# Kernel tuning notes

Hardware: AMD Instinct MI355X
Metric: run time of the kernel (lower is better)

## Reference

```python
import jax, jax.numpy as jnp
import numpy as np

TAU = 2.0        # spikingjelly LIFNode default tau
ALPHA = 4.0      # sigmoid surrogate alpha (spikingjelly default)
NUM_HEADS = 8
CHUNK = 2

@jax.custom_vjp
def heaviside(x):
    return (x >= 0).astype(x.dtype)

def _h_fwd(x):
    return heaviside(x), x

def _h_bwd(x, g):
    s = jax.nn.sigmoid(ALPHA * x)
    return (g * ALPHA * s * (1.0 - s),)

heaviside.defvjp(_h_fwd, _h_bwd)

def lif(x, v_th):
    # multi-step LIF: v <- v + (x - v)/tau ; spike = H(v - v_th) ; hard reset to 0
    def step(v, xt):
        v = v + (xt - v) / TAU
        s = heaviside(v - v_th)
        return v * (1.0 - s), s
    _, spikes = jax.lax.scan(step, jnp.zeros_like(x[0]), x)
    return spikes

def bn(x, p, eps=1e-5):
    # eval-mode BatchNorm1d over channel dim C of [T,B,C,V]; p = [gamma,beta,mean,var] each [C]
    g, b, m, v = p[0], p[1], p[2], p[3]
    scale = g * jax.lax.rsqrt(v + eps)
    return (x - m[:, None]) * scale[:, None] + b[:, None]

def setup_inputs() -> dict:
    key = jax.random.key(0)
    T, B, C, V = 8, 16, 256, 1024
    ks = jax.random.split(key, 10)
    def mk_bn(k):
        k1, k2, k3, k4 = jax.random.split(k, 4)
        return jnp.stack([
            jax.random.uniform(k1, (C,)) + 0.5,          # gamma
            0.1 * jax.random.normal(k2, (C,)),           # beta
            0.1 * jax.random.normal(k3, (C,)),           # running mean
            jax.random.uniform(k4, (C,)) * 0.5 + 0.5,    # running var (>0)
        ])
    w_scale = C ** -0.5
    return {
        "x": jax.random.normal(ks[0], (T, B, C, V), jnp.float32),
        "q_w": w_scale * jax.random.normal(ks[1], (C, C), jnp.float32),
        "k_w": w_scale * jax.random.normal(ks[2], (C, C), jnp.float32),
        "v_w": w_scale * jax.random.normal(ks[3], (C, C), jnp.float32),
        "proj_w": w_scale * jax.random.normal(ks[4], (C, C), jnp.float32),
        "proj_b": 0.01 * jax.random.normal(ks[5], (C,), jnp.float32),
        "bn_q": mk_bn(ks[6]),
        "bn_k": mk_bn(ks[7]),
        "bn_v": mk_bn(ks[8]),
        "bn_proj": mk_bn(ks[9]),
    }

def reference(x, q_w, k_w, v_w, proj_w, proj_b, bn_q, bn_k, bn_v, bn_proj):
    T, B, C, V = x.shape
    H = NUM_HEADS
    D = C // H
    N = V
    NC = T // CHUNK
    identity = x

    xs = lif(x, 1.0)  # shortcut_lif

    def branch(w, bnp):
        y = jnp.einsum('oc,tbcv->tbov', w, xs)   # 1x1 conv
        y = lif(bn(y, bnp), 1.0)
        # [T,B,C,V] -> [T,B,H,N,D]
        return y.transpose(0, 1, 3, 2).reshape(T, B, N, H, D).transpose(0, 1, 3, 2, 4)

    q = branch(q_w, bn_q)
    k = branch(k_w, bn_k)
    v = branch(v_w, bn_v)

    def chunk(t):
        # [T,B,H,N,D] -> [NC,B,H,CHUNK*N,D]
        return (t.reshape(NC, CHUNK, B, H, N, D)
                 .transpose(0, 2, 3, 1, 4, 5)
                 .reshape(NC, B, H, CHUNK * N, D))

    qc, kc, vc = chunk(q), chunk(k), chunk(v)
    attn = jnp.einsum('nbhld,nbhle->nbhde', kc, vc) * (1.0 / N)  # [NC,B,H,D,D]
    out = jnp.einsum('nbhld,nbhde->nbhle', qc, attn)             # [NC,B,H,CHUNK*N,D]
    out = (out.reshape(NC, B, H, CHUNK, N, D)
              .transpose(0, 3, 1, 2, 4, 5)
              .reshape(T, B, H, N, D))

    y = out.transpose(0, 1, 2, 4, 3).reshape(T, B, C, N)  # [T,B,H,D,N] -> [T,B,C,N]
    y = lif(y, 0.5)  # attn_lif
    y = jnp.einsum('oc,tbcv->tbov', proj_w, y) + proj_b[None, None, :, None]
    y = bn(y, bn_proj)
    return y + identity, v
```

## Files before the change

kernel.cpp:

```cpp
#include <hip/hip_runtime.h>
#include <hip/hip_bf16.h>
#include <math.h>

typedef __bf16 bf16_t;
typedef __bf16 bf16x8 __attribute__((ext_vector_type(8)));
typedef __bf16 bf16x4 __attribute__((ext_vector_type(4)));
typedef float  f32x4  __attribute__((ext_vector_type(4)));

#define T_ 8
#define B_ 16
#define C_ 256
#define V_ 1024
#define H_ 8
#define D_ 32

#define MFMA __builtin_amdgcn_mfma_f32_16x16x32_bf16

__global__ __launch_bounds__(256) void k0_split(const float* __restrict__ W,
                                                bf16_t* __restrict__ S0,
                                                bf16_t* __restrict__ S1,
                                                bf16_t* __restrict__ S2)
{
    int i = (blockIdx.x * 256 + threadIdx.x) * 4;
    float4 w = *(const float4*)(W + i);
    float wv[4] = {w.x, w.y, w.z, w.w};
    bf16x4 s0, s1, s2;
#pragma unroll
    for (int j = 0; j < 4; j++) {
        bf16_t a = (bf16_t)wv[j];
        float r1 = wv[j] - (float)a;
        bf16_t b = (bf16_t)r1;
        float r2 = r1 - (float)b;
        bf16_t c = (bf16_t)r2;
        s0[j] = a; s1[j] = b; s2[j] = c;
    }
    *(bf16x4*)(S0 + i) = s0;
    *(bf16x4*)(S1 + i) = s1;
    *(bf16x4*)(S2 + i) = s2;
}

__global__ __launch_bounds__(256) void k1_lif_tr(const float* __restrict__ x,
                                                 bf16_t* __restrict__ xsT)
{
    __shared__ bf16_t tile[64 * 72];
    const int v0 = blockIdx.x * 64, c0 = blockIdx.y * 64, b = blockIdx.z;
    const int tid = threadIdx.x;
    const int cc = tid >> 2, v16 = (tid & 3) * 16;
    const int vr = tid >> 2, c16 = (tid & 3) * 16;
    float mem[16];
#pragma unroll
    for (int j = 0; j < 16; j++) mem[j] = 0.0f;

    for (int t = 0; t < T_; t++) {
        const float* xp = x + (((size_t)(t * B_ + b) * C_ + (c0 + cc)) * V_ + v0 + v16);
        float xv[16];
#pragma unroll
        for (int q = 0; q < 4; q++) {
            float4 f = *(const float4*)(xp + q * 4);
            xv[q * 4 + 0] = f.x; xv[q * 4 + 1] = f.y;
            xv[q * 4 + 2] = f.z; xv[q * 4 + 3] = f.w;
        }
#pragma unroll
        for (int j = 0; j < 16; j++) {
            float m = mem[j];
            float d = xv[j] - m;
            m = m + d * 0.5f;
            float s = (m >= 1.0f) ? 1.0f : 0.0f;
            tile[(v16 + j) * 72 + cc] = (bf16_t)s;
            mem[j] = (s != 0.0f) ? 0.0f : m;
        }
        __syncthreads();
        bf16_t* op = xsT + (((size_t)(t * B_ + b) * V_ + (v0 + vr)) * C_ + c0 + c16);
        *(bf16x8*)op       = *(const bf16x8*)&tile[vr * 72 + c16];
        *(bf16x8*)(op + 8) = *(const bf16x8*)&tile[vr * 72 + c16 + 8];
        __syncthreads();
    }
}

template <int ORIENT>
__global__ __launch_bounds__(256, 2) void k_branch(const bf16_t* __restrict__ Wsp,
                                                   const float* __restrict__ bnp,
                                                   const bf16_t* __restrict__ xsT,
                                                   bf16_t* __restrict__ outp, float vth)
{
    __shared__ bf16_t Wl[3][64 * 40];
    __shared__ bf16_t Xl[8][64 * 40];
    __shared__ float bsc[64], bmn[64], bbt[64];
    const int v0 = blockIdx.x * 64, o0 = blockIdx.y * 64, b = blockIdx.z;
    const int tid = threadIdx.x;
    const int w = tid >> 6, l = tid & 63, lq = l >> 4, lr = l & 15;
    const int msub = (w >> 1) * 32, nsub = (w & 1) * 32;

    if (tid < 64) {
        int o = o0 + tid;
        float g = bnp[o], be = bnp[C_ + o];
        float mn = bnp[2 * C_ + o], vr2 = bnp[3 * C_ + o];
        bsc[tid] = g * (1.0f / sqrtf(vr2 + 1e-5f));
        bmn[tid] = mn; bbt[tid] = be;
    }

    f32x4 acc[8][4];
#pragma unroll
    for (int t = 0; t < 8; t++)
#pragma unroll
        for (int i = 0; i < 4; i++) acc[t][i] = (f32x4){0.f, 0.f, 0.f, 0.f};

    for (int kq = 0; kq < 8; kq++) {
        __syncthreads();
#pragma unroll
        for (int i = 0; i < 3; i++) {
            int ch = tid + i * 256;
            int lvl = ch >> 8, rem = ch & 255;
            int row = rem >> 2, col8 = (rem & 3) * 8;
            *(bf16x8*)&Wl[lvl][row * 40 + col8] =
                *(const bf16x8*)&Wsp[lvl * 65536 + (o0 + row) * 256 + kq * 32 + col8];
        }
#pragma unroll
        for (int i = 0; i < 8; i++) {
            int ch = tid + i * 256;
            int tt = ch >> 8, rem = ch & 255;
            int row = rem >> 2, col8 = (rem & 3) * 8;
            *(bf16x8*)&Xl[tt][row * 40 + col8] =
                *(const bf16x8*)&xsT[((size_t)(tt * B_ + b) * V_ + v0 + row) * C_ + kq * 32 + col8];
        }
        __syncthreads();

        bf16x8 aw0[3], aw1[3];
#pragma unroll
        for (int lvl = 0; lvl < 3; lvl++) {
            aw0[lvl] = *(const bf16x8*)&Wl[lvl][(msub + lr) * 40 + lq * 8];
            aw1[lvl] = *(const bf16x8*)&Wl[lvl][(msub + 16 + lr) * 40 + lq * 8];
        }
#pragma unroll
        for (int t = 0; t < 8; t++) {
            bf16x8 b0 = *(const bf16x8*)&Xl[t][(nsub + lr) * 40 + lq * 8];
            bf16x8 b1 = *(const bf16x8*)&Xl[t][(nsub + 16 + lr) * 40 + lq * 8];
#pragma unroll
            for (int lvl = 0; lvl < 3; lvl++) {
                if (ORIENT == 0) {
                    acc[t][0] = MFMA(aw0[lvl], b0, acc[t][0], 0, 0, 0);
                    acc[t][1] = MFMA(aw0[lvl], b1, acc[t][1], 0, 0, 0);
                    acc[t][2] = MFMA(aw1[lvl], b0, acc[t][2], 0, 0, 0);
                    acc[t][3] = MFMA(aw1[lvl], b1, acc[t][3], 0, 0, 0);
                } else {
                    acc[t][0] = MFMA(b0, aw0[lvl], acc[t][0], 0, 0, 0);
                    acc[t][1] = MFMA(b1, aw0[lvl], acc[t][1], 0, 0, 0);
                    acc[t][2] = MFMA(b0, aw1[lvl], acc[t][2], 0, 0, 0);
                    acc[t][3] = MFMA(b1, aw1[lvl], acc[t][3], 0, 0, 0);
                }
            }
        }
    }

    float mem[4][4];
#pragma unroll
    for (int st = 0; st < 4; st++)
#pragma unroll
        for (int r = 0; r < 4; r++) mem[st][r] = 0.0f;
#pragma unroll
    for (int t = 0; t < 8; t++) {
#pragma unroll
        for (int st = 0; st < 4; st++) {
            int mi = st >> 1, ni = st & 1;
#pragma unroll
            for (int r = 0; r < 4; r++) {
                int m, n;
                if (ORIENT == 0) {
                    m = msub + mi * 16 + lq * 4 + r;
                    n = nsub + ni * 16 + lr;
                } else {
                    m = msub + mi * 16 + lr;
                    n = nsub + ni * 16 + lq * 4 + r;
                }
                float y = (acc[t][st][r] - bmn[m]) * bsc[m] + bbt[m];
                float mm = mem[st][r];
                mm = mm + (y - mm) * 0.5f;
                float s = (mm >= vth) ? 1.0f : 0.0f;
                size_t idx = ORIENT
                    ? (((size_t)(t * B_ + b) * V_ + (v0 + n)) * C_ + (o0 + m))
                    : (((size_t)(t * B_ + b) * C_ + (o0 + m)) * V_ + (v0 + n));
                outp[idx] = (bf16_t)s;
                mem[st][r] = (s != 0.0f) ? 0.0f : mm;
            }
        }
    }
}

__global__ __launch_bounds__(256) void k_attn(const bf16_t* __restrict__ vc,
                                              const bf16_t* __restrict__ kc,
                                              bf16_t* __restrict__ ahi,
                                              bf16_t* __restrict__ alo)
{
    __shared__ float red[3][64][20];
    const int fid = blockIdx.x;
    const int h = fid & 7, b = (fid >> 3) & 15, nc = fid >> 7;
    const int tid = threadIdx.x, w = tid >> 6, l = tid & 63, lq = l >> 4, lr = l & 15;
    f32x4 acc[4];
#pragma unroll
    for (int i = 0; i < 4; i++) acc[i] = (f32x4){0.f, 0.f, 0.f, 0.f};
    for (int ss = 0; ss < 16; ss++) {
        int s = w * 16 + ss;
        int t = nc * 2 + (s >> 5);
        int n0 = (s & 31) * 32;
        size_t rb = ((size_t)(t * B_ + b) * C_ + h * D_ + lr) * V_ + n0 + lq * 8;
        bf16x8 a0 = *(const bf16x8*)&vc[rb];
        bf16x8 a1 = *(const bf16x8*)&vc[rb + (size_t)16 * V_];
        bf16x8 b0 = *(const bf16x8*)&kc[rb];
        bf16x8 b1 = *(const bf16x8*)&kc[rb + (size_t)16 * V_];
        acc[0] = MFMA(a0, b0, acc[0], 0, 0, 0);
        acc[1] = MFMA(a0, b1, acc[1], 0, 0, 0);
        acc[2] = MFMA(a1, b0, acc[2], 0, 0, 0);
        acc[3] = MFMA(a1, b1, acc[3], 0, 0, 0);
    }
    if (w) {
#pragma unroll
        for (int st = 0; st < 4; st++)
            *(f32x4*)&red[w - 1][l][st * 4] = acc[st];
    }
    __syncthreads();
    if (w == 0) {
#pragma unroll
        for (int st = 0; st < 4; st++)
#pragma unroll
            for (int i = 0; i < 3; i++)
                acc[st] += *(const f32x4*)&red[i][l][st * 4];

        size_t ob = (size_t)fid * 1024;
#pragma unroll
        for (int st = 0; st < 4; st++) {
            int ei = st >> 1, di = st & 1;
#pragma unroll
            for (int r = 0; r < 4; r++) {
                int e = ei * 16 + lq * 4 + r;
                int d = di * 16 + lr;
                float val = acc[st][r] * (1.0f / 1024.0f);
                bf16_t hi = (bf16_t)val;
                float lo = val - (float)hi;
                ahi[ob + e * 32 + d] = hi;
                alo[ob + e * 32 + d] = (bf16_t)lo;
            }
        }
    }
}

__global__ __launch_bounds__(256) void k_attn_out(const bf16_t* __restrict__ qT,
                                                  const bf16_t* __restrict__ ahi,
                                                  const bf16_t* __restrict__ alo,
                                                  bf16_t* __restrict__ y3T)
{
    const int tid = threadIdx.x, w = tid >> 6, l = tid & 63, lq = l >> 4, lr = l & 15;
    const int n0 = blockIdx.x * 64 + (w >> 1) * 32;
    const int h = blockIdx.y * 2 + (w & 1);
    const int b = blockIdx.z;
    float mem[4][4];
#pragma unroll
    for (int st = 0; st < 4; st++)
#pragma unroll
        for (int r = 0; r < 4; r++) mem[st][r] = 0.0f;

    for (int t = 0; t < T_; t++) {
        int nc = t >> 1;
        const bf16_t* qp = qT + ((size_t)(t * B_ + b) * V_ + n0 + lr) * C_ + h * D_ + lq * 8;
        bf16x8 a0 = *(const bf16x8*)qp;
        bf16x8 a1 = *(const bf16x8*)(qp + 16 * C_);
        size_t ab = ((size_t)(nc * B_ + b) * H_ + h) * 1024;
        bf16x8 bh0 = *(const bf16x8*)&ahi[ab + lr * 32 + lq * 8];
        bf16x8 bh1 = *(const bf16x8*)&ahi[ab + (16 + lr) * 32 + lq * 8];
        bf16x8 bl0 = *(const bf16x8*)&alo[ab + lr * 32 + lq * 8];
        bf16x8 bl1 = *(const bf16x8*)&alo[ab + (16 + lr) * 32 + lq * 8];
#pragma unroll
        for (int st = 0; st < 4; st++) {
            int mi = st >> 1, ni = st & 1;
            f32x4 z = (f32x4){0.f, 0.f, 0.f, 0.f};
            z = MFMA(mi ? a1 : a0, ni ? bh1 : bh0, z, 0, 0, 0);
            z = MFMA(mi ? a1 : a0, ni ? bl1 : bl0, z, 0, 0, 0);
#pragma unroll
            for (int r = 0; r < 4; r++) {
                int n = n0 + mi * 16 + lq * 4 + r;
                int e = ni * 16 + lr;
                float mm = mem[st][r];
                mm = mm + (z[r] - mm) * 0.5f;
                float s = (mm >= 0.5f) ? 1.0f : 0.0f;
                y3T[((size_t)(t * B_ + b) * V_ + n) * C_ + h * D_ + e] = (bf16_t)s;
                mem[st][r] = (s != 0.0f) ? 0.0f : mm;
            }
        }
    }
}

__global__ __launch_bounds__(256, 2) void k_proj(const bf16_t* __restrict__ Wsp,
                                                 const float* __restrict__ pb,
                                                 const float* __restrict__ bnp,
                                                 const bf16_t* __restrict__ y3T,
                                                 const float* __restrict__ x,
                                                 float* __restrict__ out0)
{
    __shared__ bf16_t Wl[3][64 * 40];
    __shared__ bf16_t Xl[8][64 * 40];
    __shared__ float bsc[64], bmn[64], bbt[64], bbi[64];
    const int v0 = blockIdx.x * 64, o0 = blockIdx.y * 64, b = blockIdx.z;
    const int tid = threadIdx.x;
    const int w = tid >> 6, l = tid & 63, lq = l >> 4, lr = l & 15;
    const int msub = (w >> 1) * 32, nsub = (w & 1) * 32;

    if (tid < 64) {
        int o = o0 + tid;
        float g = bnp[o], be = bnp[C_ + o];
        float mn = bnp[2 * C_ + o], vr2 = bnp[3 * C_ + o];
        bsc[tid] = g * (1.0f / sqrtf(vr2 + 1e-5f));
        bmn[tid] = mn; bbt[tid] = be; bbi[tid] = pb[o];
    }

    f32x4 acc[8][4];
#pragma unroll
    for (int t = 0; t < 8; t++)
#pragma unroll
        for (int i = 0; i < 4; i++) acc[t][i] = (f32x4){0.f, 0.f, 0.f, 0.f};

    for (int kq = 0; kq < 8; kq++) {
        __syncthreads();
#pragma unroll
        for (int i = 0; i < 3; i++) {
            int ch = tid + i * 256;
            int lvl = ch >> 8, rem = ch & 255;
            int row = rem >> 2, col8 = (rem & 3) * 8;
            *(bf16x8*)&Wl[lvl][row * 40 + col8] =
                *(const bf16x8*)&Wsp[lvl * 65536 + (o0 + row) * 256 + kq * 32 + col8];
        }
#pragma unroll
        for (int i = 0; i < 8; i++) {
            int ch = tid + i * 256;
            int tt = ch >> 8, rem = ch & 255;
            int row = rem >> 2, col8 = (rem & 3) * 8;
            *(bf16x8*)&Xl[tt][row * 40 + col8] =
                *(const bf16x8*)&y3T[((size_t)(tt * B_ + b) * V_ + v0 + row) * C_ + kq * 32 + col8];
        }
        __syncthreads();

        bf16x8 aw0[3], aw1[3];
#pragma unroll
        for (int lvl = 0; lvl < 3; lvl++) {
            aw0[lvl] = *(const bf16x8*)&Wl[lvl][(msub + lr) * 40 + lq * 8];
            aw1[lvl] = *(const bf16x8*)&Wl[lvl][(msub + 16 + lr) * 40 + lq * 8];
        }
#pragma unroll
        for (int t = 0; t < 8; t++) {
            bf16x8 b0 = *(const bf16x8*)&Xl[t][(nsub + lr) * 40 + lq * 8];
            bf16x8 b1 = *(const bf16x8*)&Xl[t][(nsub + 16 + lr) * 40 + lq * 8];
#pragma unroll
            for (int lvl = 0; lvl < 3; lvl++) {
                acc[t][0] = MFMA(aw0[lvl], b0, acc[t][0], 0, 0, 0);
                acc[t][1] = MFMA(aw0[lvl], b1, acc[t][1], 0, 0, 0);
                acc[t][2] = MFMA(aw1[lvl], b0, acc[t][2], 0, 0, 0);
                acc[t][3] = MFMA(aw1[lvl], b1, acc[t][3], 0, 0, 0);
            }
        }
    }

#pragma unroll
    for (int t = 0; t < 8; t++) {
#pragma unroll
        for (int st = 0; st < 4; st++) {
            int mi = st >> 1, ni = st & 1;
#pragma unroll
            for (int r = 0; r < 4; r++) {
                int m = msub + mi * 16 + lq * 4 + r;
                int n = nsub + ni * 16 + lr;
                size_t idx = ((size_t)(t * B_ + b) * C_ + (o0 + m)) * V_ + (v0 + n);
                float y = acc[t][st][r] + bbi[m];
                y = (y - bmn[m]) * bsc[m] + bbt[m];
                y += x[idx];
                out0[idx] = y;
            }
        }
    }
}

__global__ __launch_bounds__(256) void k_vout(const bf16_t* __restrict__ vc,
                                              float* __restrict__ out1)
{
    __shared__ bf16_t tl[32 * 136];
    const int n0 = blockIdx.x * 128;
    const int f = blockIdx.y;
    const int tb = f >> 3, h = f & 7;
    const int tid = threadIdx.x;
    {
        int d = tid >> 3, nn = (tid & 7) * 16;
        const bf16_t* vp = vc + ((size_t)tb * C_ + h * D_ + d) * V_ + n0 + nn;
        *(bf16x8*)&tl[d * 136 + nn]     = *(const bf16x8*)vp;
        *(bf16x8*)&tl[d * 136 + nn + 8] = *(const bf16x8*)(vp + 8);
    }
    __syncthreads();
    {
        int n = tid >> 1, d16 = (tid & 1) * 16;
        float* op = out1 + (size_t)f * (V_ * D_) + (size_t)(n0 + n) * D_ + d16;
#pragma unroll
        for (int q = 0; q < 4; q++) {
            float4 o;
            o.x = (float)tl[(d16 + q * 4 + 0) * 136 + n];
            o.y = (float)tl[(d16 + q * 4 + 1) * 136 + n];
            o.z = (float)tl[(d16 + q * 4 + 2) * 136 + n];
            o.w = (float)tl[(d16 + q * 4 + 3) * 136 + n];
            *(float4*)(op + q * 4) = o;
        }
    }
}

extern "C" void kernel_launch(void* const* d_in, const int* in_sizes, int n_in,
                              void* d_out, int out_size, void* d_ws, size_t ws_size,
                              hipStream_t stream)
{
    const float* x    = (const float*)d_in[0];
    const float* q_w  = (const float*)d_in[1];
    const float* k_w  = (const float*)d_in[2];
    const float* v_w  = (const float*)d_in[3];
    const float* pw   = (const float*)d_in[4];
    const float* pb   = (const float*)d_in[5];
    const float* bn_q = (const float*)d_in[6];
    const float* bn_k = (const float*)d_in[7];
    const float* bn_v = (const float*)d_in[8];
    const float* bn_p = (const float*)d_in[9];

    char* ws = (char*)d_ws;
    bf16_t* xsT  = (bf16_t*)(ws);
    bf16_t* vc   = (bf16_t*)(ws + ((size_t)64 << 20));
    bf16_t* ahi  = (bf16_t*)(ws + ((size_t)128 << 20));
    bf16_t* alo  = (bf16_t*)(ws + ((size_t)129 << 20));
    bf16_t* wspq = (bf16_t*)(ws + ((size_t)130 << 20));
    bf16_t* wspk = wspq + 3 * 65536;
    bf16_t* wspv = wspk + 3 * 65536;
    bf16_t* wspp = wspv + 3 * 65536;
    bf16_t* y3T  = xsT;

    float* outf = (float*)d_out;
    bf16_t* qT = (bf16_t*)d_out;
    bf16_t* kc = (bf16_t*)((char*)d_out + ((size_t)64 << 20));

    k0_split<<<dim3(64), 256, 0, stream>>>(q_w, wspq, wspq + 65536, wspq + 131072);
    k0_split<<<dim3(64), 256, 0, stream>>>(k_w, wspk, wspk + 65536, wspk + 131072);
    k0_split<<<dim3(64), 256, 0, stream>>>(v_w, wspv, wspv + 65536, wspv + 131072);
    k0_split<<<dim3(64), 256, 0, stream>>>(pw,  wspp, wspp + 65536, wspp + 131072);

    k1_lif_tr   <<<dim3(16, 4, 16),  256, 0, stream>>>(x, xsT);
    k_branch<1> <<<dim3(16, 4, 16),  256, 0, stream>>>(wspq, bn_q, xsT, qT, 1.0f);
    k_branch<0> <<<dim3(16, 4, 16),  256, 0, stream>>>(wspk, bn_k, xsT, kc, 1.0f);
    k_branch<0> <<<dim3(16, 4, 16),  256, 0, stream>>>(wspv, bn_v, xsT, vc, 1.0f);
    k_attn      <<<dim3(512),        256, 0, stream>>>(vc, kc, ahi, alo);
    k_attn_out  <<<dim3(16, 4, 16),  256, 0, stream>>>(qT, ahi, alo, y3T);
    k_proj      <<<dim3(16, 4, 16),  256, 0, stream>>>(wspp, pb, bn_p, y3T, x, outf);
    k_vout      <<<dim3(8, 1024),    256, 0, stream>>>(vc, outf + (size_t)33554432);
}
```

Baseline: 712.6 us.

## Prefetch GEMM tiles into registers, fuse v output into branch, merge split kernels

The branch and proj GEMM kernels now load the next K-slice of weights and activations into registers while the current slice is computed from shared memory, overlapping global loads with MFMA work. The v branch kernel also writes the fp32 v output directly through a shared-memory transpose, which removes the separate k_vout pass that re-read vc. The four weight-split launches are merged into one. The cost is higher register pressure from holding 11 bf16x8 staging vectors under launch_bounds(256,2), plus extra syncs inside the v kernel's per-timestep epilogue.

```diff
diff --git a/kernel.cpp b/kernel.cpp
--- a/kernel.cpp
+++ b/kernel.cpp
@@ -16,12 +16,18 @@
 
 #define MFMA __builtin_amdgcn_mfma_f32_16x16x32_bf16
 
-__global__ __launch_bounds__(256) void k0_split(const float* __restrict__ W,
-                                                bf16_t* __restrict__ S0,
-                                                bf16_t* __restrict__ S1,
-                                                bf16_t* __restrict__ S2)
-{
-    int i = (blockIdx.x * 256 + threadIdx.x) * 4;
+__global__ __launch_bounds__(256) void k0_split4(const float* __restrict__ W0,
+                                                 const float* __restrict__ W1,
+                                                 const float* __restrict__ W2,
+                                                 const float* __restrict__ W3,
+                                                 bf16_t* __restrict__ S)
+{
+    const int mat = blockIdx.x >> 6;
+    const float* W = (mat == 0) ? W0 : (mat == 1) ? W1 : (mat == 2) ? W2 : W3;
+    bf16_t* S0 = S + (size_t)mat * 3 * 65536;
+    bf16_t* S1 = S0 + 65536;
+    bf16_t* S2 = S0 + 131072;
+    int i = ((blockIdx.x & 63) * 256 + threadIdx.x) * 4;
     float4 w = *(const float4*)(W + i);
     float wv[4] = {w.x, w.y, w.z, w.w};
     bf16x4 s0, s1, s2;
@@ -77,11 +83,12 @@
     }
 }
 
-template <int ORIENT>
+template <int ORIENT, int VOUT>
 __global__ __launch_bounds__(256, 2) void k_branch(const bf16_t* __restrict__ Wsp,
                                                    const float* __restrict__ bnp,
                                                    const bf16_t* __restrict__ xsT,
-                                                   bf16_t* __restrict__ outp, float vth)
+                                                   bf16_t* __restrict__ outp, float vth,
+                                                   float* __restrict__ out1)
 {
     __shared__ bf16_t Wl[3][64 * 40];
     __shared__ bf16_t Xl[8][64 * 40];
@@ -105,25 +112,50 @@
 #pragma unroll
         for (int i = 0; i < 4; i++) acc[t][i] = (f32x4){0.f, 0.f, 0.f, 0.f};
 
+    bf16x8 wst[3], xst[8];
+#pragma unroll
+    for (int i = 0; i < 3; i++) {
+        int ch = tid + i * 256, lvl = ch >> 8, rem = ch & 255;
+        int row = rem >> 2, col8 = (rem & 3) * 8;
+        wst[i] = *(const bf16x8*)&Wsp[lvl * 65536 + (o0 + row) * 256 + col8];
+    }
+#pragma unroll
+    for (int i = 0; i < 8; i++) {
+        int ch = tid + i * 256, tt = ch >> 8, rem = ch & 255;
+        int row = rem >> 2, col8 = (rem & 3) * 8;
+        xst[i] = *(const bf16x8*)&xsT[((size_t)(tt * B_ + b) * V_ + v0 + row) * C_ + col8];
+    }
+
     for (int kq = 0; kq < 8; kq++) {
         __syncthreads();
 #pragma unroll
         for (int i = 0; i < 3; i++) {
-            int ch = tid + i * 256;
-            int lvl = ch >> 8, rem = ch & 255;
+            int ch = tid + i * 256, lvl = ch >> 8, rem = ch & 255;
             int row = rem >> 2, col8 = (rem & 3) * 8;
-            *(bf16x8*)&Wl[lvl][row * 40 + col8] =
-                *(const bf16x8*)&Wsp[lvl * 65536 + (o0 + row) * 256 + kq * 32 + col8];
+            *(bf16x8*)&Wl[lvl][row * 40 + col8] = wst[i];
         }
 #pragma unroll
         for (int i = 0; i < 8; i++) {
-            int ch = tid + i * 256;
-            int tt = ch >> 8, rem = ch & 255;
+            int ch = tid + i * 256, tt = ch >> 8, rem = ch & 255;
             int row = rem >> 2, col8 = (rem & 3) * 8;
-            *(bf16x8*)&Xl[tt][row * 40 + col8] =
-                *(const bf16x8*)&xsT[((size_t)(tt * B_ + b) * V_ + v0 + row) * C_ + kq * 32 + col8];
-        }
-        __syncthreads();
+            *(bf16x8*)&Xl[tt][row * 40 + col8] = xst[i];
+        }
+        __syncthreads();
+        if (kq < 7) {
+            int kc8 = (kq + 1) * 32;
+#pragma unroll
+            for (int i = 0; i < 3; i++) {
+                int ch = tid + i * 256, lvl = ch >> 8, rem = ch & 255;
+                int row = rem >> 2, col8 = (rem & 3) * 8;
+                wst[i] = *(const bf16x8*)&Wsp[lvl * 65536 + (o0 + row) * 256 + kc8 + col8];
+            }
+#pragma unroll
+            for (int i = 0; i < 8; i++) {
+                int ch = tid + i * 256, tt = ch >> 8, rem = ch & 255;
+                int row = rem >> 2, col8 = (rem & 3) * 8;
+                xst[i] = *(const bf16x8*)&xsT[((size_t)(tt * B_ + b) * V_ + v0 + row) * C_ + kc8 + col8];
+            }
+        }
 
         bf16x8 aw0[3], aw1[3];
 #pragma unroll
@@ -152,6 +184,8 @@
         }
     }
 
+    bf16_t* tl = (bf16_t*)Xl;
+    if (VOUT) __syncthreads();
     float mem[4][4];
 #pragma unroll
     for (int st = 0; st < 4; st++)
@@ -181,7 +215,25 @@
                     : (((size_t)(t * B_ + b) * C_ + (o0 + m)) * V_ + (v0 + n));
                 outp[idx] = (bf16_t)s;
                 mem[st][r] = (s != 0.0f) ? 0.0f : mm;
-            }
+                if (VOUT) tl[n * 66 + m] = (bf16_t)s;
+            }
+        }
+        if (VOUT) {
+            __syncthreads();
+            int nn = tid & 63, ho = tid >> 6;
+            int h = (o0 >> 5) + (ho >> 1), d16 = (ho & 1) * 16;
+            float* op = out1 + ((size_t)((t * B_ + b) * H_ + h)) * (V_ * D_)
+                             + (size_t)(v0 + nn) * D_ + d16;
+#pragma unroll
+            for (int q2 = 0; q2 < 4; q2++) {
+                float4 o4;
+                o4.x = (float)tl[nn * 66 + ho * 16 + q2 * 4 + 0];
+                o4.y = (float)tl[nn * 66 + ho * 16 + q2 * 4 + 1];
+                o4.z = (float)tl[nn * 66 + ho * 16 + q2 * 4 + 2];
+                o4.w = (float)tl[nn * 66 + ho * 16 + q2 * 4 + 3];
+                *(float4*)(op + q2 * 4) = o4;
+            }
+            __syncthreads();
         }
     }
 }
@@ -317,25 +369,50 @@
 #pragma unroll
         for (int i = 0; i < 4; i++) acc[t][i] = (f32x4){0.f, 0.f, 0.f, 0.f};
 
+    bf16x8 wst[3], xst[8];
+#pragma unroll
+    for (int i = 0; i < 3; i++) {
+        int ch = tid + i * 256, lvl = ch >> 8, rem = ch & 255;
+        int row = rem >> 2, col8 = (rem & 3) * 8;
+        wst[i] = *(const bf16x8*)&Wsp[lvl * 65536 + (o0 + row) * 256 + col8];
+    }
+#pragma unroll
+    for (int i = 0; i < 8; i++) {
+        int ch = tid + i * 256, tt = ch >> 8, rem = ch & 255;
+        int row = rem >> 2, col8 = (rem & 3) * 8;
+        xst[i] = *(const bf16x8*)&y3T[((size_t)(tt * B_ + b) * V_ + v0 + row) * C_ + col8];
+    }
+
     for (int kq = 0; kq < 8; kq++) {
         __syncthreads();
 #pragma unroll
         for (int i = 0; i < 3; i++) {
-            int ch = tid + i * 256;
-            int lvl = ch >> 8, rem = ch & 255;
+            int ch = tid + i * 256, lvl = ch >> 8, rem = ch & 255;
             int row = rem >> 2, col8 = (rem & 3) * 8;
-            *(bf16x8*)&Wl[lvl][row * 40 + col8] =
-                *(const bf16x8*)&Wsp[lvl * 65536 + (o0 + row) * 256 + kq * 32 + col8];
+            *(bf16x8*)&Wl[lvl][row * 40 + col8] = wst[i];
         }
 #pragma unroll
         for (int i = 0; i < 8; i++) {
-            int ch = tid + i * 256;
-            int tt = ch >> 8, rem = ch & 255;
+            int ch = tid + i * 256, tt = ch >> 8, rem = ch & 255;
             int row = rem >> 2, col8 = (rem & 3) * 8;
-            *(bf16x8*)&Xl[tt][row * 40 + col8] =
-                *(const bf16x8*)&y3T[((size_t)(tt * B_ + b) * V_ + v0 + row) * C_ + kq * 32 + col8];
-        }
-        __syncthreads();
+            *(bf16x8*)&Xl[tt][row * 40 + col8] = xst[i];
+        }
+        __syncthreads();
+        if (kq < 7) {
+            int kc8 = (kq + 1) * 32;
+#pragma unroll
+            for (int i = 0; i < 3; i++) {
+                int ch = tid + i * 256, lvl = ch >> 8, rem = ch & 255;
+                int row = rem >> 2, col8 = (rem & 3) * 8;
+                wst[i] = *(const bf16x8*)&Wsp[lvl * 65536 + (o0 + row) * 256 + kc8 + col8];
+            }
+#pragma unroll
+            for (int i = 0; i < 8; i++) {
+                int ch = tid + i * 256, tt = ch >> 8, rem = ch & 255;
+                int row = rem >> 2, col8 = (rem & 3) * 8;
+                xst[i] = *(const bf16x8*)&y3T[((size_t)(tt * B_ + b) * V_ + v0 + row) * C_ + kc8 + col8];
+            }
+        }
 
         bf16x8 aw0[3], aw1[3];
 #pragma unroll
@@ -372,36 +449,6 @@
                 y += x[idx];
                 out0[idx] = y;
             }
-        }
-    }
-}
-
-__global__ __launch_bounds__(256) void k_vout(const bf16_t* __restrict__ vc,
-                                              float* __restrict__ out1)
-{
-    __shared__ bf16_t tl[32 * 136];
-    const int n0 = blockIdx.x * 128;
-    const int f = blockIdx.y;
-    const int tb = f >> 3, h = f & 7;
-    const int tid = threadIdx.x;
-    {
-        int d = tid >> 3, nn = (tid & 7) * 16;
-        const bf16_t* vp = vc + ((size_t)tb * C_ + h * D_ + d) * V_ + n0 + nn;
-        *(bf16x8*)&tl[d * 136 + nn]     = *(const bf16x8*)vp;
-        *(bf16x8*)&tl[d * 136 + nn + 8] = *(const bf16x8*)(vp + 8);
-    }
-    __syncthreads();
-    {
-        int n = tid >> 1, d16 = (tid & 1) * 16;
-        float* op = out1 + (size_t)f * (V_ * D_) + (size_t)(n0 + n) * D_ + d16;
-#pragma unroll
-        for (int q = 0; q < 4; q++) {
-            float4 o;
-            o.x = (float)tl[(d16 + q * 4 + 0) * 136 + n];
-            o.y = (float)tl[(d16 + q * 4 + 1) * 136 + n];
-            o.z = (float)tl[(d16 + q * 4 + 2) * 136 + n];
-            o.w = (float)tl[(d16 + q * 4 + 3) * 136 + n];
-            *(float4*)(op + q * 4) = o;
         }
     }
 }
@@ -433,20 +480,16 @@
     bf16_t* y3T  = xsT;
 
     float* outf = (float*)d_out;
+    float* out1 = outf + (size_t)33554432;
     bf16_t* qT = (bf16_t*)d_out;
     bf16_t* kc = (bf16_t*)((char*)d_out + ((size_t)64 << 20));
 
-    k0_split<<<dim3(64), 256, 0, stream>>>(q_w, wspq, wspq + 65536, wspq + 131072);
-    k0_split<<<dim3(64), 256, 0, stream>>>(k_w, wspk, wspk + 65536, wspk + 131072);
-    k0_split<<<dim3(64), 256, 0, stream>>>(v_w, wspv, wspv + 65536, wspv + 131072);
-    k0_split<<<dim3(64), 256, 0, stream>>>(pw,  wspp, wspp + 65536, wspp + 131072);
-
-    k1_lif_tr   <<<dim3(16, 4, 16),  256, 0, stream>>>(x, xsT);
-    k_branch<1> <<<dim3(16, 4, 16),  256, 0, stream>>>(wspq, bn_q, xsT, qT, 1.0f);
-    k_branch<0> <<<dim3(16, 4, 16),  256, 0, stream>>>(wspk, bn_k, xsT, kc, 1.0f);
-    k_branch<0> <<<dim3(16, 4, 16),  256, 0, stream>>>(wspv, bn_v, xsT, vc, 1.0f);
-    k_attn      <<<dim3(512),        256, 0, stream>>>(vc, kc, ahi, alo);
-    k_attn_out  <<<dim3(16, 4, 16),  256, 0, stream>>>(qT, ahi, alo, y3T);
-    k_proj      <<<dim3(16, 4, 16),  256, 0, stream>>>(wspp, pb, bn_p, y3T, x, outf);
-    k_vout      <<<dim3(8, 1024),    256, 0, stream>>>(vc, outf + (size_t)33554432);
-}
+    k0_split4   <<<dim3(256),       256, 0, stream>>>(q_w, k_w, v_w, pw, wspq);
+    k1_lif_tr   <<<dim3(16, 4, 16), 256, 0, stream>>>(x, xsT);
+    k_branch<1,0><<<dim3(16, 4, 16),256, 0, stream>>>(wspq, bn_q, xsT, qT, 1.0f, nullptr);
+    k_branch<0,0><<<dim3(16, 4, 16),256, 0, stream>>>(wspk, bn_k, xsT, kc, 1.0f, nullptr);
+    k_branch<0,1><<<dim3(16, 4, 16),256, 0, stream>>>(wspv, bn_v, xsT, vc, 1.0f, out1);
+    k_attn      <<<dim3(512),       256, 0, stream>>>(vc, kc, ahi, alo);
+    k_attn_out  <<<dim3(16, 4, 16), 256, 0, stream>>>(qT, ahi, alo, y3T);
+    k_proj      <<<dim3(16, 4, 16), 256, 0, stream>>>(wspp, pb, bn_p, y3T, x, outf);
+}
```

New measurement: 764.1 us. 1.07x slower.

## Widen GEMM blocks to 512 threads, fuse v-output into branch, merge weight splits

Applied to the files above, without the earlier changes.

The branch and projection GEMM kernels now run 8 waves per block, each computing a 32x16 sub-tile instead of 32x32. The intent is to halve per-thread accumulators and raise occupancy, at the cost of more LDS fragment reloads per MFMA. The v-branch kernel writes the fp32 [T,B,H,N,D] v output directly through an LDS transpose, which removes the separate k_vout pass that re-read vc. The four weight-split launches are merged into one kernel. The fused v output adds extra barriers per timestep inside the v-branch kernel.

```diff
diff --git a/kernel.cpp b/kernel.cpp
--- a/kernel.cpp
+++ b/kernel.cpp
@@ -16,12 +16,18 @@
 
 #define MFMA __builtin_amdgcn_mfma_f32_16x16x32_bf16
 
-__global__ __launch_bounds__(256) void k0_split(const float* __restrict__ W,
-                                                bf16_t* __restrict__ S0,
-                                                bf16_t* __restrict__ S1,
-                                                bf16_t* __restrict__ S2)
-{
-    int i = (blockIdx.x * 256 + threadIdx.x) * 4;
+__global__ __launch_bounds__(256) void k0_split4(const float* __restrict__ W0,
+                                                 const float* __restrict__ W1,
+                                                 const float* __restrict__ W2,
+                                                 const float* __restrict__ W3,
+                                                 bf16_t* __restrict__ S)
+{
+    const int mat = blockIdx.x >> 6;
+    const float* W = (mat == 0) ? W0 : (mat == 1) ? W1 : (mat == 2) ? W2 : W3;
+    bf16_t* S0 = S + (size_t)mat * 3 * 65536;
+    bf16_t* S1 = S0 + 65536;
+    bf16_t* S2 = S0 + 131072;
+    int i = ((blockIdx.x & 63) * 256 + threadIdx.x) * 4;
     float4 w = *(const float4*)(W + i);
     float wv[4] = {w.x, w.y, w.z, w.w};
     bf16x4 s0, s1, s2;
@@ -77,11 +83,12 @@
     }
 }
 
-template <int ORIENT>
-__global__ __launch_bounds__(256, 2) void k_branch(const bf16_t* __restrict__ Wsp,
+template <int ORIENT, int VOUT>
+__global__ __launch_bounds__(512, 4) void k_branch(const bf16_t* __restrict__ Wsp,
                                                    const float* __restrict__ bnp,
                                                    const bf16_t* __restrict__ xsT,
-                                                   bf16_t* __restrict__ outp, float vth)
+                                                   bf16_t* __restrict__ outp, float vth,
+                                                   float* __restrict__ out1)
 {
     __shared__ bf16_t Wl[3][64 * 40];
     __shared__ bf16_t Xl[8][64 * 40];
@@ -89,7 +96,7 @@
     const int v0 = blockIdx.x * 64, o0 = blockIdx.y * 64, b = blockIdx.z;
     const int tid = threadIdx.x;
     const int w = tid >> 6, l = tid & 63, lq = l >> 4, lr = l & 15;
-    const int msub = (w >> 1) * 32, nsub = (w & 1) * 32;
+    const int msub = (w >> 2) * 32, nsub = (w & 3) * 16;
 
     if (tid < 64) {
         int o = o0 + tid;
@@ -99,26 +106,27 @@
         bmn[tid] = mn; bbt[tid] = be;
     }
 
-    f32x4 acc[8][4];
-#pragma unroll
-    for (int t = 0; t < 8; t++)
-#pragma unroll
-        for (int i = 0; i < 4; i++) acc[t][i] = (f32x4){0.f, 0.f, 0.f, 0.f};
+    f32x4 acc[8][2];
+#pragma unroll
+    for (int t = 0; t < 8; t++) {
+        acc[t][0] = (f32x4){0.f, 0.f, 0.f, 0.f};
+        acc[t][1] = (f32x4){0.f, 0.f, 0.f, 0.f};
+    }
 
     for (int kq = 0; kq < 8; kq++) {
         __syncthreads();
-#pragma unroll
-        for (int i = 0; i < 3; i++) {
-            int ch = tid + i * 256;
-            int lvl = ch >> 8, rem = ch & 255;
-            int row = rem >> 2, col8 = (rem & 3) * 8;
-            *(bf16x8*)&Wl[lvl][row * 40 + col8] =
-                *(const bf16x8*)&Wsp[lvl * 65536 + (o0 + row) * 256 + kq * 32 + col8];
-        }
-#pragma unroll
-        for (int i = 0; i < 8; i++) {
-            int ch = tid + i * 256;
-            int tt = ch >> 8, rem = ch & 255;
+        if (tid < 384) {
+#pragma unroll
+            for (int i = 0; i < 2; i++) {
+                int ch = tid + i * 384, lvl = ch >> 8, rem = ch & 255;
+                int row = rem >> 2, col8 = (rem & 3) * 8;
+                *(bf16x8*)&Wl[lvl][row * 40 + col8] =
+                    *(const bf16x8*)&Wsp[lvl * 65536 + (o0 + row) * 256 + kq * 32 + col8];
+            }
+        }
+#pragma unroll
+        for (int i = 0; i < 4; i++) {
+            int ch = tid + i * 512, tt = ch >> 8, rem = ch & 255;
             int row = rem >> 2, col8 = (rem & 3) * 8;
             *(bf16x8*)&Xl[tt][row * 40 + col8] =
                 *(const bf16x8*)&xsT[((size_t)(tt * B_ + b) * V_ + v0 + row) * C_ + kq * 32 + col8];
@@ -133,55 +141,71 @@
         }
 #pragma unroll
         for (int t = 0; t < 8; t++) {
-            bf16x8 b0 = *(const bf16x8*)&Xl[t][(nsub + lr) * 40 + lq * 8];
-            bf16x8 b1 = *(const bf16x8*)&Xl[t][(nsub + 16 + lr) * 40 + lq * 8];
+            bf16x8 bx = *(const bf16x8*)&Xl[t][(nsub + lr) * 40 + lq * 8];
 #pragma unroll
             for (int lvl = 0; lvl < 3; lvl++) {
                 if (ORIENT == 0) {
-                    acc[t][0] = MFMA(aw0[lvl], b0, acc[t][0], 0, 0, 0);
-                    acc[t][1] = MFMA(aw0[lvl], b1, acc[t][1], 0, 0, 0);
-                    acc[t][2] = MFMA(aw1[lvl], b0, acc[t][2], 0, 0, 0);
-                    acc[t][3] = MFMA(aw1[lvl], b1, acc[t][3], 0, 0, 0);
+                    acc[t][0] = MFMA(aw0[lvl], bx, acc[t][0], 0, 0, 0);
+                    acc[t][1] = MFMA(aw1[lvl], bx, acc[t][1], 0, 0, 0);
                 } else {
-                    acc[t][0] = MFMA(b0, aw0[lvl], acc[t][0], 0, 0, 0);
-                    acc[t][1] = MFMA(b1, aw0[lvl], acc[t][1], 0, 0, 0);
-                    acc[t][2] = MFMA(b0, aw1[lvl], acc[t][2], 0, 0, 0);
-                    acc[t][3] = MFMA(b1, aw1[lvl], acc[t][3], 0, 0, 0);
+                    acc[t][0] = MFMA(bx, aw0[lvl], acc[t][0], 0, 0, 0);
+                    acc[t][1] = MFMA(bx, aw1[lvl], acc[t][1], 0, 0, 0);
                 }
             }
         }
     }
 
-    float mem[4][4];
-#pragma unroll
-    for (int st = 0; st < 4; st++)
-#pragma unroll
-        for (int r = 0; r < 4; r++) mem[st][r] = 0.0f;
+    bf16_t* tl = (bf16_t*)Xl;
+    if (VOUT) __syncthreads();
+    float mem[2][4];
+#pragma unroll
+    for (int mi = 0; mi < 2; mi++)
+#pragma unroll
+        for (int r = 0; r < 4; r++) mem[mi][r] = 0.0f;
 #pragma unroll
     for (int t = 0; t < 8; t++) {
 #pragma unroll
-        for (int st = 0; st < 4; st++) {
-            int mi = st >> 1, ni = st & 1;
+        for (int mi = 0; mi < 2; mi++) {
 #pragma unroll
             for (int r = 0; r < 4; r++) {
                 int m, n;
                 if (ORIENT == 0) {
                     m = msub + mi * 16 + lq * 4 + r;
-                    n = nsub + ni * 16 + lr;
+                    n = nsub + lr;
                 } else {
                     m = msub + mi * 16 + lr;
-                    n = nsub + ni * 16 + lq * 4 + r;
+                    n = nsub + lq * 4 + r;
                 }
-                float y = (acc[t][st][r] - bmn[m]) * bsc[m] + bbt[m];
-                float mm = mem[st][r];
+                float y = (acc[t][mi][r] - bmn[m]) * bsc[m] + bbt[m];
+                float mm = mem[mi][r];
                 mm = mm + (y - mm) * 0.5f;
                 float s = (mm >= vth) ? 1.0f : 0.0f;
                 size_t idx = ORIENT
                     ? (((size_t)(t * B_ + b) * V_ + (v0 + n)) * C_ + (o0 + m))
                     : (((size_t)(t * B_ + b) * C_ + (o0 + m)) * V_ + (v0 + n));
                 outp[idx] = (bf16_t)s;
-                mem[st][r] = (s != 0.0f) ? 0.0f : mm;
-            }
+                mem[mi][r] = (s != 0.0f) ? 0.0f : mm;
+                if (VOUT) tl[n * 66 + m] = (bf16_t)s;
+            }
+        }
+        if (VOUT) {
+            __syncthreads();
+            int nn = tid & 63, og = tid >> 6;
+            int o_base = og * 8;
+            int h = (o0 >> 5) + (o_base >> 5);
+            int d0 = o_base & 31;
+            float* op = out1 + ((size_t)((t * B_ + b) * H_ + h)) * (V_ * D_)
+                             + (size_t)(v0 + nn) * D_ + d0;
+#pragma unroll
+            for (int q2 = 0; q2 < 2; q2++) {
+                float4 o4;
+                o4.x = (float)tl[nn * 66 + o_base + q2 * 4 + 0];
+                o4.y = (float)tl[nn * 66 + o_base + q2 * 4 + 1];
+                o4.z = (float)tl[nn * 66 + o_base + q2 * 4 + 2];
+                o4.w = (float)tl[nn * 66 + o_base + q2 * 4 + 3];
+                *(float4*)(op + q2 * 4) = o4;
+            }
+            __syncthreads();
         }
     }
 }
@@ -288,7 +312,7 @@
     }
 }
 
-__global__ __launch_bounds__(256, 2) void k_proj(const bf16_t* __restrict__ Wsp,
+__global__ __launch_bounds__(512, 4) void k_proj(const bf16_t* __restrict__ Wsp,
                                                  const float* __restrict__ pb,
                                                  const float* __restrict__ bnp,
                                                  const bf16_t* __restrict__ y3T,
@@ -301,7 +325,7 @@
     const int v0 = blockIdx.x * 64, o0 = blockIdx.y * 64, b = blockIdx.z;
     const int tid = threadIdx.x;
     const int w = tid >> 6, l = tid & 63, lq = l >> 4, lr = l & 15;
-    const int msub = (w >> 1) * 32, nsub = (w & 1) * 32;
+    const int msub = (w >> 2) * 32, nsub = (w & 3) * 16;
 
     if (tid < 64) {
         int o = o0 + tid;
@@ -311,26 +335,27 @@
         bmn[tid] = mn; bbt[tid] = be; bbi[tid] = pb[o];
     }
 
-    f32x4 acc[8][4];
-#pragma unroll
-    for (int t = 0; t < 8; t++)
-#pragma unroll
-        for (int i = 0; i < 4; i++) acc[t][i] = (f32x4){0.f, 0.f, 0.f, 0.f};
+    f32x4 acc[8][2];
+#pragma unroll
+    for (int t = 0; t < 8; t++) {
+        acc[t][0] = (f32x4){0.f, 0.f, 0.f, 0.f};
+        acc[t][1] = (f32x4){0.f, 0.f, 0.f, 0.f};
+    }
 
     for (int kq = 0; kq < 8; kq++) {
         __syncthreads();
-#pragma unroll
-        for (int i = 0; i < 3; i++) {
-            int ch = tid + i * 256;
-            int lvl = ch >> 8, rem = ch & 255;
-            int row = rem >> 2, col8 = (rem & 3) * 8;
-            *(bf16x8*)&Wl[lvl][row * 40 + col8] =
-                *(const bf16x8*)&Wsp[lvl * 65536 + (o0 + row) * 256 + kq * 32 + col8];
-        }
-#pragma unroll
-        for (int i = 0; i < 8; i++) {
-            int ch = tid + i * 256;
-            int tt = ch >> 8, rem = ch & 255;
+        if (tid < 384) {
+#pragma unroll
+            for (int i = 0; i < 2; i++) {
+                int ch = tid + i * 384, lvl = ch >> 8, rem = ch & 255;
+                int row = rem >> 2, col8 = (rem & 3) * 8;
+                *(bf16x8*)&Wl[lvl][row * 40 + col8] =
+                    *(const bf16x8*)&Wsp[lvl * 65536 + (o0 + row) * 256 + kq * 32 + col8];
+            }
+        }
+#pragma unroll
+        for (int i = 0; i < 4; i++) {
+            int ch = tid + i * 512, tt = ch >> 8, rem = ch & 255;
             int row = rem >> 2, col8 = (rem & 3) * 8;
             *(bf16x8*)&Xl[tt][row * 40 + col8] =
                 *(const bf16x8*)&y3T[((size_t)(tt * B_ + b) * V_ + v0 + row) * C_ + kq * 32 + col8];
@@ -345,14 +370,11 @@
         }
 #pragma unroll
         for (int t = 0; t < 8; t++) {
-            bf16x8 b0 = *(const bf16x8*)&Xl[t][(nsub + lr) * 40 + lq * 8];
-            bf16x8 b1 = *(const bf16x8*)&Xl[t][(nsub + 16 + lr) * 40 + lq * 8];
+            bf16x8 bx = *(const bf16x8*)&Xl[t][(nsub + lr) * 40 + lq * 8];
 #pragma unroll
             for (int lvl = 0; lvl < 3; lvl++) {
-                acc[t][0] = MFMA(aw0[lvl], b0, acc[t][0], 0, 0, 0);
-                acc[t][1] = MFMA(aw0[lvl], b1, acc[t][1], 0, 0, 0);
-                acc[t][2] = MFMA(aw1[lvl], b0, acc[t][2], 0, 0, 0);
-                acc[t][3] = MFMA(aw1[lvl], b1, acc[t][3], 0, 0, 0);
+                acc[t][0] = MFMA(aw0[lvl], bx, acc[t][0], 0, 0, 0);
+                acc[t][1] = MFMA(aw1[lvl], bx, acc[t][1], 0, 0, 0);
             }
         }
     }
@@ -360,48 +382,17 @@
 #pragma unroll
     for (int t = 0; t < 8; t++) {
 #pragma unroll
-        for (int st = 0; st < 4; st++) {
-            int mi = st >> 1, ni = st & 1;
+        for (int mi = 0; mi < 2; mi++) {
 #pragma unroll
             for (int r = 0; r < 4; r++) {
                 int m = msub + mi * 16 + lq * 4 + r;
-                int n = nsub + ni * 16 + lr;
+                int n = nsub + lr;
                 size_t idx = ((size_t)(t * B_ + b) * C_ + (o0 + m)) * V_ + (v0 + n);
-                float y = acc[t][st][r] + bbi[m];
+                float y = acc[t][mi][r] + bbi[m];
                 y = (y - bmn[m]) * bsc[m] + bbt[m];
                 y += x[idx];
                 out0[idx] = y;
             }
-        }
-    }
-}
-
-__global__ __launch_bounds__(256) void k_vout(const bf16_t* __restrict__ vc,
-                                              float* __restrict__ out1)
-{
-    __shared__ bf16_t tl[32 * 136];
-    const int n0 = blockIdx.x * 128;
-    const int f = blockIdx.y;
-    const int tb = f >> 3, h = f & 7;
-    const int tid = threadIdx.x;
-    {
-        int d = tid >> 3, nn = (tid & 7) * 16;
-        const bf16_t* vp = vc + ((size_t)tb * C_ + h * D_ + d) * V_ + n0 + nn;
-        *(bf16x8*)&tl[d * 136 + nn]     = *(const bf16x8*)vp;
-        *(bf16x8*)&tl[d * 136 + nn + 8] = *(const bf16x8*)(vp + 8);
-    }
-    __syncthreads();
-    {
-        int n = tid >> 1, d16 = (tid & 1) * 16;
-        float* op = out1 + (size_t)f * (V_ * D_) + (size_t)(n0 + n) * D_ + d16;
-#pragma unroll
-        for (int q = 0; q < 4; q++) {
-            float4 o;
-            o.x = (float)tl[(d16 + q * 4 + 0) * 136 + n];
-            o.y = (float)tl[(d16 + q * 4 + 1) * 136 + n];
-            o.z = (float)tl[(d16 + q * 4 + 2) * 136 + n];
-            o.w = (float)tl[(d16 + q * 4 + 3) * 136 + n];
-            *(float4*)(op + q * 4) = o;
         }
     }
 }
@@ -433,20 +424,16 @@
     bf16_t* y3T  = xsT;
 
     float* outf = (float*)d_out;
+    float* out1 = outf + (size_t)33554432;
     bf16_t* qT = (bf16_t*)d_out;
     bf16_t* kc = (bf16_t*)((char*)d_out + ((size_t)64 << 20));
 
-    k0_split<<<dim3(64), 256, 0, stream>>>(q_w, wspq, wspq + 65536, wspq + 131072);
-    k0_split<<<dim3(64), 256, 0, stream>>>(k_w, wspk, wspk + 65536, wspk + 131072);
-    k0_split<<<dim3(64), 256, 0, stream>>>(v_w, wspv, wspv + 65536, wspv + 131072);
-    k0_split<<<dim3(64), 256, 0, stream>>>(pw,  wspp, wspp + 65536, wspp + 131072);
-
-    k1_lif_tr   <<<dim3(16, 4, 16),  256, 0, stream>>>(x, xsT);
-    k_branch<1> <<<dim3(16, 4, 16),  256, 0, stream>>>(wspq, bn_q, xsT, qT, 1.0f);
-    k_branch<0> <<<dim3(16, 4, 16),  256, 0, stream>>>(wspk, bn_k, xsT, kc, 1.0f);
-    k_branch<0> <<<dim3(16, 4, 16),  256, 0, stream>>>(wspv, bn_v, xsT, vc, 1.0f);
-    k_attn      <<<dim3(512),        256, 0, stream>>>(vc, kc, ahi, alo);
-    k_attn_out  <<<dim3(16, 4, 16),  256, 0, stream>>>(qT, ahi, alo, y3T);
-    k_proj      <<<dim3(16, 4, 16),  256, 0, stream>>>(wspp, pb, bn_p, y3T, x, outf);
-    k_vout      <<<dim3(8, 1024),    256, 0, stream>>>(vc, outf + (size_t)33554432);
-}
+    k0_split4   <<<dim3(256),       256, 0, stream>>>(q_w, k_w, v_w, pw, wspq);
+    k1_lif_tr   <<<dim3(16, 4, 16), 256, 0, stream>>>(x, xsT);
+    k_branch<1,0><<<dim3(16, 4, 16),512, 0, stream>>>(wspq, bn_q, xsT, qT, 1.0f, nullptr);
+    k_branch<0,0><<<dim3(16, 4, 16),512, 0, stream>>>(wspk, bn_k, xsT, kc, 1.0f, nullptr);
+    k_branch<0,1><<<dim3(16, 4, 16),512, 0, stream>>>(wspv, bn_v, xsT, vc, 1.0f, out1);
+    k_attn      <<<dim3(512),       256, 0, stream>>>(vc, kc, ahi, alo);
+    k_attn_out  <<<dim3(16, 4, 16), 256, 0, stream>>>(qT, ahi, alo, y3T);
+    k_proj      <<<dim3(16, 4, 16), 512, 0, stream>>>(wspp, pb, bn_p, y3T, x, outf);
+}
```

Result: slower. 813.1 us (+14.1%).
